# Kernel tuning notes

Hardware: AMD Instinct MI355X
Metric: run time of the kernel (lower is better)

Reference implementation:

```python
import jax, jax.numpy as jnp
import numpy as np

E4M3 = jnp.float8_e4m3fn  # HPU e4m3 (max 240) approximated by e4m3fn grid
E5M2 = jnp.float8_e5m2


def fp8_quant_dequant(x, scale, dt):
    # cast_to_fp8(x, scale) followed by inline dequant (1/scale) inside fp8_gemm_v2
    return (x * scale).astype(dt).astype(jnp.float32) / scale


def setup_inputs() -> dict:
    key = jax.random.key(0)
    k1, k2 = jax.random.split(key)
    A, B, C, OUT = 4, 2048, 2048, 8192
    return {
        "input": jax.random.normal(k1, (A, B, C), jnp.float32),
        "weight": jax.random.normal(k2, (OUT, C), jnp.float32) * 0.02,
        "input_scale_e4m3": jnp.ones((), jnp.float32),
        "weight_scale_e4m3": jnp.ones((), jnp.float32),
        "input_scale_e5m2": jnp.ones((), jnp.float32),
        "weight_scale_e5m2": jnp.ones((), jnp.float32),
        "grad_scale_e5m2": jnp.ones((), jnp.float32),
    }


def reference(input, weight, input_scale_e4m3, weight_scale_e4m3,
              input_scale_e5m2, weight_scale_e5m2, grad_scale_e5m2):
    A, B, C = input.shape
    x2d = input.reshape(A * B, C)
    # forward path uses the e4m3 copies from cast_to_fp8_hybrid
    x_q = fp8_quant_dequant(x2d, input_scale_e4m3, E4M3)      # [A*B, C]
    w_q = fp8_quant_dequant(weight, weight_scale_e4m3, E4M3)  # [OUT, C]
    out = x_q @ w_q.T                                          # [A*B, OUT]
    return out.reshape(A, B, -1)
```

## Files before the change

kernel.cpp:

```cpp
#include <hip/hip_runtime.h>

typedef float floatx16 __attribute__((ext_vector_type(16)));
typedef int   intx4    __attribute__((ext_vector_type(4)));
typedef int   intx8    __attribute__((ext_vector_type(8)));

#define GEMM_M 8192
#define GEMM_N 8192
#define GEMM_K 2048

__global__ __launch_bounds__(256) void quant_e4m3(const float* __restrict__ x,
                                                  const float* __restrict__ scale,
                                                  int4* __restrict__ q)
{
    const int i = blockIdx.x * blockDim.x + threadIdx.x;
    const float s = scale[0];
    const float4* __restrict__ x4 = (const float4*)x;
    float4 v0 = x4[i * 4 + 0];
    float4 v1 = x4[i * 4 + 1];
    float4 v2 = x4[i * 4 + 2];
    float4 v3 = x4[i * 4 + 3];
    int4 r;
    int p;
    p = __builtin_amdgcn_cvt_pk_fp8_f32(v0.x * s, v0.y * s, 0, false);
    p = __builtin_amdgcn_cvt_pk_fp8_f32(v0.z * s, v0.w * s, p, true);
    r.x = p;
    p = __builtin_amdgcn_cvt_pk_fp8_f32(v1.x * s, v1.y * s, 0, false);
    p = __builtin_amdgcn_cvt_pk_fp8_f32(v1.z * s, v1.w * s, p, true);
    r.y = p;
    p = __builtin_amdgcn_cvt_pk_fp8_f32(v2.x * s, v2.y * s, 0, false);
    p = __builtin_amdgcn_cvt_pk_fp8_f32(v2.z * s, v2.w * s, p, true);
    r.z = p;
    p = __builtin_amdgcn_cvt_pk_fp8_f32(v3.x * s, v3.y * s, 0, false);
    p = __builtin_amdgcn_cvt_pk_fp8_f32(v3.z * s, v3.w * s, p, true);
    r.w = p;
    q[i] = r;
}

__global__ __launch_bounds__(256) void gemm_fp8_mx(
    const unsigned char* __restrict__ Aq,
    const unsigned char* __restrict__ Bq,
    float* __restrict__ C,
    const float* __restrict__ sa,
    const float* __restrict__ sb)
{
    __shared__ __align__(16) unsigned char sA[128 * 64];
    __shared__ __align__(16) unsigned char sB[128 * 64];

    const int tid  = threadIdx.x;
    const int lane = tid & 63;
    const int wave = tid >> 6;
    const int bn   = blockIdx.x;
    const int bm   = blockIdx.y;

    const int r0   = (wave * 2 + 0) * 16 + (lane >> 2);
    const int r1   = (wave * 2 + 1) * 16 + (lane >> 2);
    const int cswz = (((lane & 3) ^ ((lane >> 3) & 3)) << 4);

    const unsigned char* gA0 = Aq + (size_t)(bm * 128 + r0) * GEMM_K + cswz;
    const unsigned char* gA1 = Aq + (size_t)(bm * 128 + r1) * GEMM_K + cswz;
    const unsigned char* gB0 = Bq + (size_t)(bn * 128 + r0) * GEMM_K + cswz;
    const unsigned char* gB1 = Bq + (size_t)(bn * 128 + r1) * GEMM_K + cswz;

    unsigned char* lA0 = &sA[(wave * 2 + 0) * 1024 + lane * 16];
    unsigned char* lA1 = &sA[(wave * 2 + 1) * 1024 + lane * 16];
    unsigned char* lB0 = &sB[(wave * 2 + 0) * 1024 + lane * 16];
    unsigned char* lB1 = &sB[(wave * 2 + 1) * 1024 + lane * 16];

    const int mloc = lane & 31;
    const int h    = lane >> 5;
    const int swz  = (mloc >> 1) & 3;
    const int wm   = wave >> 1, wn = wave & 1;

    unsigned alo[2], ahi[2], blo[2], bhi[2];
#pragma unroll
    for (int t = 0; t < 2; ++t) {
        const unsigned arow = (unsigned)(wm * 64 + t * 32 + mloc) << 6;
        const unsigned brow = (unsigned)(wn * 64 + t * 32 + mloc) << 6;
        alo[t] = arow + (((2 * h + 0) ^ swz) << 4);
        ahi[t] = arow + (((2 * h + 1) ^ swz) << 4);
        blo[t] = brow + (((2 * h + 0) ^ swz) << 4);
        bhi[t] = brow + (((2 * h + 1) ^ swz) << 4);
    }

    floatx16 acc[2][2];
#pragma unroll
    for (int i = 0; i < 2; ++i)
#pragma unroll
        for (int j = 0; j < 2; ++j)
            acc[i][j] = (floatx16)(0.0f);

    for (int kt = 0; kt < GEMM_K / 64; ++kt) {
        const int kb = kt * 64;
        __builtin_amdgcn_global_load_lds(
            (const __attribute__((address_space(1))) void*)(gA0 + kb),
            (__attribute__((address_space(3))) void*)lA0, 16, 0, 0);
        __builtin_amdgcn_global_load_lds(
            (const __attribute__((address_space(1))) void*)(gA1 + kb),
            (__attribute__((address_space(3))) void*)lA1, 16, 0, 0);
        __builtin_amdgcn_global_load_lds(
            (const __attribute__((address_space(1))) void*)(gB0 + kb),
            (__attribute__((address_space(3))) void*)lB0, 16, 0, 0);
        __builtin_amdgcn_global_load_lds(
            (const __attribute__((address_space(1))) void*)(gB1 + kb),
            (__attribute__((address_space(3))) void*)lB1, 16, 0, 0);
        __syncthreads();

        intx8 a[2], b[2];
#pragma unroll
        for (int t = 0; t < 2; ++t) {
            intx4 lo = *(const intx4*)&sA[alo[t]];
            intx4 hi = *(const intx4*)&sA[ahi[t]];
            a[t] = __builtin_shufflevector(lo, hi, 0, 1, 2, 3, 4, 5, 6, 7);
        }
#pragma unroll
        for (int t = 0; t < 2; ++t) {
            intx4 lo = *(const intx4*)&sB[blo[t]];
            intx4 hi = *(const intx4*)&sB[bhi[t]];
            b[t] = __builtin_shufflevector(lo, hi, 0, 1, 2, 3, 4, 5, 6, 7);
        }

#pragma unroll
        for (int i = 0; i < 2; ++i)
#pragma unroll
            for (int j = 0; j < 2; ++j)
                acc[i][j] = __builtin_amdgcn_mfma_scale_f32_32x32x64_f8f6f4(
                    a[i], b[j], acc[i][j],
                    0, 0,
                    0, 0x7f7f7f7f,
                    0, 0x7f7f7f7f);

        __syncthreads();
    }

    const float inv = 1.0f / (sa[0] * sb[0]);
#pragma unroll
    for (int ti = 0; ti < 2; ++ti) {
        const int row0 = bm * 128 + wm * 64 + ti * 32 + 4 * h;
#pragma unroll
        for (int tj = 0; tj < 2; ++tj) {
            const int col = bn * 128 + wn * 64 + tj * 32 + mloc;
#pragma unroll
            for (int reg = 0; reg < 16; ++reg) {
                const int row = row0 + (reg & 3) + 8 * (reg >> 2);
                C[(size_t)row * GEMM_N + col] = acc[ti][tj][reg] * inv;
            }
        }
    }
}

extern "C" void kernel_launch(void* const* d_in, const int* in_sizes, int n_in,
                              void* d_out, int out_size, void* d_ws, size_t ws_size,
                              hipStream_t stream) {
    const float* x    = (const float*)d_in[0];
    const float* w    = (const float*)d_in[1];
    const float* s_in = (const float*)d_in[2];
    const float* s_w  = (const float*)d_in[3];
    float* out = (float*)d_out;

    unsigned char* qx = (unsigned char*)d_ws;
    unsigned char* qw = qx + (size_t)GEMM_M * GEMM_K;

    const int nthr_x = in_sizes[0] / 16;
    const int nthr_w = in_sizes[1] / 16;
    quant_e4m3<<<nthr_x / 256, 256, 0, stream>>>(x, s_in, (int4*)qx);
    quant_e4m3<<<nthr_w / 256, 256, 0, stream>>>(w, s_w, (int4*)qw);

    dim3 grid(GEMM_N / 128, GEMM_M / 128);
    gemm_fp8_mx<<<grid, 256, 0, stream>>>(qx, qw, out, s_in, s_w);
}
```

Measured before the change: 485.0 us.

## Widen GEMM block tile to 128x256 and coalesce quantization loads

The GEMM block tile grows from 128x128 to 128x256. Each wave now computes a 64x128 output with 8 MFMA accumulators, which raises arithmetic intensity per LDS tile and halves how often A tiles are reloaded across N-blocks. The cost is higher register pressure (128 accumulator VGPRs plus a larger B fragment), which the occupancy hint of 2 blocks per CU bounds. The quantization kernel is rewritten so each thread handles four float4s strided by 256, making the loads and 4-byte stores coalesced across the block.

```diff
diff --git a/kernel.cpp b/kernel.cpp
--- a/kernel.cpp
+++ b/kernel.cpp
@@ -10,33 +10,22 @@
 
 __global__ __launch_bounds__(256) void quant_e4m3(const float* __restrict__ x,
                                                   const float* __restrict__ scale,
-                                                  int4* __restrict__ q)
+                                                  int* __restrict__ q)
 {
-    const int i = blockIdx.x * blockDim.x + threadIdx.x;
     const float s = scale[0];
+    const int base = blockIdx.x * 1024 + threadIdx.x;
     const float4* __restrict__ x4 = (const float4*)x;
-    float4 v0 = x4[i * 4 + 0];
-    float4 v1 = x4[i * 4 + 1];
-    float4 v2 = x4[i * 4 + 2];
-    float4 v3 = x4[i * 4 + 3];
-    int4 r;
-    int p;
-    p = __builtin_amdgcn_cvt_pk_fp8_f32(v0.x * s, v0.y * s, 0, false);
-    p = __builtin_amdgcn_cvt_pk_fp8_f32(v0.z * s, v0.w * s, p, true);
-    r.x = p;
-    p = __builtin_amdgcn_cvt_pk_fp8_f32(v1.x * s, v1.y * s, 0, false);
-    p = __builtin_amdgcn_cvt_pk_fp8_f32(v1.z * s, v1.w * s, p, true);
-    r.y = p;
-    p = __builtin_amdgcn_cvt_pk_fp8_f32(v2.x * s, v2.y * s, 0, false);
-    p = __builtin_amdgcn_cvt_pk_fp8_f32(v2.z * s, v2.w * s, p, true);
-    r.z = p;
-    p = __builtin_amdgcn_cvt_pk_fp8_f32(v3.x * s, v3.y * s, 0, false);
-    p = __builtin_amdgcn_cvt_pk_fp8_f32(v3.z * s, v3.w * s, p, true);
-    r.w = p;
-    q[i] = r;
+#pragma unroll
+    for (int j = 0; j < 4; ++j) {
+        float4 v = x4[base + j * 256];
+        int p;
+        p = __builtin_amdgcn_cvt_pk_fp8_f32(v.x * s, v.y * s, 0, false);
+        p = __builtin_amdgcn_cvt_pk_fp8_f32(v.z * s, v.w * s, p, true);
+        q[base + j * 256] = p;
+    }
 }
 
-__global__ __launch_bounds__(256) void gemm_fp8_mx(
+__global__ __launch_bounds__(256, 2) void gemm_fp8_mx(
     const unsigned char* __restrict__ Aq,
     const unsigned char* __restrict__ Bq,
     float* __restrict__ C,
@@ -44,7 +33,7 @@
     const float* __restrict__ sb)
 {
     __shared__ __align__(16) unsigned char sA[128 * 64];
-    __shared__ __align__(16) unsigned char sB[128 * 64];
+    __shared__ __align__(16) unsigned char sB[256 * 64];
 
     const int tid  = threadIdx.x;
     const int lane = tid & 63;
@@ -52,60 +41,68 @@
     const int bn   = blockIdx.x;
     const int bm   = blockIdx.y;
 
-    const int r0   = (wave * 2 + 0) * 16 + (lane >> 2);
-    const int r1   = (wave * 2 + 1) * 16 + (lane >> 2);
+    const int rseg = lane >> 2;
     const int cswz = (((lane & 3) ^ ((lane >> 3) & 3)) << 4);
 
-    const unsigned char* gA0 = Aq + (size_t)(bm * 128 + r0) * GEMM_K + cswz;
-    const unsigned char* gA1 = Aq + (size_t)(bm * 128 + r1) * GEMM_K + cswz;
-    const unsigned char* gB0 = Bq + (size_t)(bn * 128 + r0) * GEMM_K + cswz;
-    const unsigned char* gB1 = Bq + (size_t)(bn * 128 + r1) * GEMM_K + cswz;
-
-    unsigned char* lA0 = &sA[(wave * 2 + 0) * 1024 + lane * 16];
-    unsigned char* lA1 = &sA[(wave * 2 + 1) * 1024 + lane * 16];
-    unsigned char* lB0 = &sB[(wave * 2 + 0) * 1024 + lane * 16];
-    unsigned char* lB1 = &sB[(wave * 2 + 1) * 1024 + lane * 16];
+    const unsigned char* gA[2];
+    unsigned char*       lA[2];
+#pragma unroll
+    for (int t = 0; t < 2; ++t) {
+        const int s = wave * 2 + t;
+        gA[t] = Aq + (size_t)(bm * 128 + s * 16 + rseg) * GEMM_K + cswz;
+        lA[t] = &sA[s * 1024 + lane * 16];
+    }
+    const unsigned char* gB[4];
+    unsigned char*       lB[4];
+#pragma unroll
+    for (int t = 0; t < 4; ++t) {
+        const int s = wave * 4 + t;
+        gB[t] = Bq + (size_t)(bn * 256 + s * 16 + rseg) * GEMM_K + cswz;
+        lB[t] = &sB[s * 1024 + lane * 16];
+    }
 
     const int mloc = lane & 31;
     const int h    = lane >> 5;
     const int swz  = (mloc >> 1) & 3;
     const int wm   = wave >> 1, wn = wave & 1;
 
-    unsigned alo[2], ahi[2], blo[2], bhi[2];
+    unsigned alo[2], ahi[2];
 #pragma unroll
     for (int t = 0; t < 2; ++t) {
-        const unsigned arow = (unsigned)(wm * 64 + t * 32 + mloc) << 6;
-        const unsigned brow = (unsigned)(wn * 64 + t * 32 + mloc) << 6;
-        alo[t] = arow + (((2 * h + 0) ^ swz) << 4);
-        ahi[t] = arow + (((2 * h + 1) ^ swz) << 4);
-        blo[t] = brow + (((2 * h + 0) ^ swz) << 4);
-        bhi[t] = brow + (((2 * h + 1) ^ swz) << 4);
+        const unsigned row = (unsigned)(wm * 64 + t * 32 + mloc) << 6;
+        alo[t] = row + (((2 * h + 0) ^ swz) << 4);
+        ahi[t] = row + (((2 * h + 1) ^ swz) << 4);
+    }
+    unsigned blo[4], bhi[4];
+#pragma unroll
+    for (int t = 0; t < 4; ++t) {
+        const unsigned row = (unsigned)(wn * 128 + t * 32 + mloc) << 6;
+        blo[t] = row + (((2 * h + 0) ^ swz) << 4);
+        bhi[t] = row + (((2 * h + 1) ^ swz) << 4);
     }
 
-    floatx16 acc[2][2];
+    floatx16 acc[2][4];
 #pragma unroll
     for (int i = 0; i < 2; ++i)
 #pragma unroll
-        for (int j = 0; j < 2; ++j)
+        for (int j = 0; j < 4; ++j)
             acc[i][j] = (floatx16)(0.0f);
 
     for (int kt = 0; kt < GEMM_K / 64; ++kt) {
         const int kb = kt * 64;
-        __builtin_amdgcn_global_load_lds(
-            (const __attribute__((address_space(1))) void*)(gA0 + kb),
-            (__attribute__((address_space(3))) void*)lA0, 16, 0, 0);
-        __builtin_amdgcn_global_load_lds(
-            (const __attribute__((address_space(1))) void*)(gA1 + kb),
-            (__attribute__((address_space(3))) void*)lA1, 16, 0, 0);
-        __builtin_amdgcn_global_load_lds(
-            (const __attribute__((address_space(1))) void*)(gB0 + kb),
-            (__attribute__((address_space(3))) void*)lB0, 16, 0, 0);
-        __builtin_amdgcn_global_load_lds(
-            (const __attribute__((address_space(1))) void*)(gB1 + kb),
-            (__attribute__((address_space(3))) void*)lB1, 16, 0, 0);
+#pragma unroll
+        for (int t = 0; t < 2; ++t)
+            __builtin_amdgcn_global_load_lds(
+                (const __attribute__((address_space(1))) void*)(gA[t] + kb),
+                (__attribute__((address_space(3))) void*)lA[t], 16, 0, 0);
+#pragma unroll
+        for (int t = 0; t < 4; ++t)
+            __builtin_amdgcn_global_load_lds(
+                (const __attribute__((address_space(1))) void*)(gB[t] + kb),
+                (__attribute__((address_space(3))) void*)lB[t], 16, 0, 0);
         __syncthreads();
 
-        intx8 a[2], b[2];
+        intx8 a[2], b[4];
 #pragma unroll
         for (int t = 0; t < 2; ++t) {
             intx4 lo = *(const intx4*)&sA[alo[t]];
@@ -113,7 +110,7 @@
             a[t] = __builtin_shufflevector(lo, hi, 0, 1, 2, 3, 4, 5, 6, 7);
         }
 #pragma unroll
-        for (int t = 0; t < 2; ++t) {
+        for (int t = 0; t < 4; ++t) {
             intx4 lo = *(const intx4*)&sB[blo[t]];
             intx4 hi = *(const intx4*)&sB[bhi[t]];
             b[t] = __builtin_shufflevector(lo, hi, 0, 1, 2, 3, 4, 5, 6, 7);
@@ -122,7 +119,7 @@
 #pragma unroll
         for (int i = 0; i < 2; ++i)
 #pragma unroll
-            for (int j = 0; j < 2; ++j)
+            for (int j = 0; j < 4; ++j)
                 acc[i][j] = __builtin_amdgcn_mfma_scale_f32_32x32x64_f8f6f4(
                     a[i], b[j], acc[i][j],
                     0, 0,
@@ -137,8 +134,8 @@
     for (int ti = 0; ti < 2; ++ti) {
         const int row0 = bm * 128 + wm * 64 + ti * 32 + 4 * h;
 #pragma unroll
-        for (int tj = 0; tj < 2; ++tj) {
-            const int col = bn * 128 + wn * 64 + tj * 32 + mloc;
+        for (int tj = 0; tj < 4; ++tj) {
+            const int col = bn * 256 + wn * 128 + tj * 32 + mloc;
 #pragma unroll
             for (int reg = 0; reg < 16; ++reg) {
                 const int row = row0 + (reg & 3) + 8 * (reg >> 2);
@@ -160,11 +157,9 @@
     unsigned char* qx = (unsigned char*)d_ws;
     unsigned char* qw = qx + (size_t)GEMM_M * GEMM_K;
 
-    const int nthr_x = in_sizes[0] / 16;
-    const int nthr_w = in_sizes[1] / 16;
-    quant_e4m3<<<nthr_x / 256, 256, 0, stream>>>(x, s_in, (int4*)qx);
-    quant_e4m3<<<nthr_w / 256, 256, 0, stream>>>(w, s_w, (int4*)qw);
+    quant_e4m3<<<in_sizes[0] / 4096, 256, 0, stream>>>(x, s_in, (int*)qx);
+    quant_e4m3<<<in_sizes[1] / 4096, 256, 0, stream>>>(w, s_w, (int*)qw);
 
-    dim3 grid(GEMM_N / 128, GEMM_M / 128);
+    dim3 grid(GEMM_N / 256, GEMM_M / 128);
     gemm_fp8_mx<<<grid, 256, 0, stream>>>(qx, qw, out, s_in, s_w);
 }
```

After: 484.6 us. Within noise of the previous version (-0.1%).
